# Performance work log

Hardware: AMD Instinct MI355X
Metric: run time of the kernel (lower is better)

The kernel has to match this reference:

```python
import jax, jax.numpy as jnp
import numpy as np

N = 20000          # n_nodes
E = 320000         # n_edges (before self loops)
F_IN, H1, H2 = 256, 64, 32
HEADS = 5
NEG_SLOPE = 0.2    # PyG GATConv leaky_relu default


def setup_inputs() -> dict:
    key = jax.random.key(0)
    ks = jax.random.split(key, 16)
    g = lambda i, shape, s: (jax.random.normal(ks[i], shape, jnp.float32) * s)
    inp = {
        "x": g(0, (N, F_IN), 1.0),
        "edge_index": jax.random.randint(ks[1], (2, E), 0, N, dtype=jnp.int32),
        "W1": g(2, (F_IN, HEADS * H1), 0.05),
        "att_src1": g(3, (HEADS, H1), 0.1),
        "att_dst1": g(4, (HEADS, H1), 0.1),
        "b1": jnp.zeros((H1,), jnp.float32),
        "W2": g(5, (H1, HEADS * H2), 0.1),
        "att_src2": g(6, (HEADS, H2), 0.1),
        "att_dst2": g(7, (HEADS, H2), 0.1),
        "b2": jnp.zeros((H2,), jnp.float32),
        "W3": g(8, (H1, HEADS * H2), 0.1),
        "att_src3": g(9, (HEADS, H2), 0.1),
        "att_dst3": g(10, (HEADS, H2), 0.1),
        "b3": jnp.zeros((H2,), jnp.float32),
    }
    return inp


def _add_self_loops(edge_index):
    loop = jnp.arange(N, dtype=edge_index.dtype)
    return jnp.concatenate([edge_index, jnp.stack([loop, loop])], axis=1)


def _gat_conv(x, edge_index, W, att_src, att_dst, b, act):
    # PyG GATConv, concat=False (mean over heads), add_self_loops already applied.
    heads, c = att_src.shape
    xw = (x @ W).reshape(N, heads, c)                     # [N,H,C]
    src, dst = edge_index[0], edge_index[1]               # messages src -> dst
    a_s = jnp.sum(xw * att_src, axis=-1)                  # [N,H]
    a_d = jnp.sum(xw * att_dst, axis=-1)                  # [N,H]
    e = jax.nn.leaky_relu(a_s[src] + a_d[dst], NEG_SLOPE) # [E',H]
    # scatter-softmax over edges sharing the same destination node
    m = jax.ops.segment_max(e, dst, num_segments=N)       # [N,H]
    e = jnp.exp(e - m[dst])
    denom = jax.ops.segment_sum(e, dst, num_segments=N)   # [N,H]
    alpha = e / (denom[dst] + 1e-16)                      # [E',H]
    # weighted scatter-aggregation of gathered source features
    out = jax.ops.segment_sum(alpha[:, :, None] * xw[src], dst, num_segments=N)
    out = out.mean(axis=1) + b                            # mean over heads, bias
    return act(out)


def reference(x, edge_index, W1, att_src1, att_dst1, b1,
              W2, att_src2, att_dst2, b2,
              W3, att_src3, att_dst3, b3):
    ei = _add_self_loops(edge_index)
    h1 = _gat_conv(x, ei, W1, att_src1, att_dst1, b1, jax.nn.relu)
    mu = _gat_conv(h1, ei, W2, att_src2, att_dst2, b2, lambda t: t)
    logvar = _gat_conv(h1, ei, W3, att_src3, att_dst3, b3, lambda t: t)
    z = mu  # eval-mode reparameterize: z = mu
    return (z, mu, logvar)
```

## Files before the change

### kernel.cpp

```cpp
#include <hip/hip_runtime.h>
#include <math.h>

#define N_NODES 20000
#define N_EDGES 320000
#define EP (N_EDGES + N_NODES)
#define HEADS 5

typedef __attribute__((ext_vector_type(8))) __bf16 bf16x8;
typedef __attribute__((ext_vector_type(4))) float f32x4;

__device__ __forceinline__ float lrelu(float s) { return (s > 0.f) ? s : 0.2f * s; }

__device__ __forceinline__ unsigned f2bf(float f) {
  unsigned u = __float_as_uint(f);
  return (u + 0x7fffu + ((u >> 16) & 1u)) >> 16;
}

__global__ void count_deg_k(const int* __restrict__ ei, int* __restrict__ deg) {
  int e = blockIdx.x * blockDim.x + threadIdx.x;
  if (e >= EP) return;
  int dst = (e < N_EDGES) ? ei[N_EDGES + e] : (e - N_EDGES);
  atomicAdd(&deg[dst], 1);
}

__global__ __launch_bounds__(256) void scan1_k(const int* __restrict__ deg,
                                               int* __restrict__ offs,
                                               int* __restrict__ bsum) {
  __shared__ int buf[256];
  int tid = threadIdx.x, i = blockIdx.x * 256 + tid;
  int v = (i < N_NODES) ? deg[i] : 0;
  buf[tid] = v;
  __syncthreads();
  for (int o = 1; o < 256; o <<= 1) {
    int t = (tid >= o) ? buf[tid - o] : 0;
    __syncthreads();
    buf[tid] += t;
    __syncthreads();
  }
  if (i < N_NODES) offs[i] = buf[tid] - v;
  if (tid == 255) bsum[blockIdx.x] = buf[255];
}

__global__ __launch_bounds__(128) void scan2_k(int* __restrict__ bsum, int nb) {
  __shared__ int buf[128];
  int tid = threadIdx.x;
  int v = (tid < nb) ? bsum[tid] : 0;
  buf[tid] = v;
  __syncthreads();
  for (int o = 1; o < 128; o <<= 1) {
    int t = (tid >= o) ? buf[tid - o] : 0;
    __syncthreads();
    buf[tid] += t;
    __syncthreads();
  }
  if (tid < nb) bsum[tid] = buf[tid] - v;
}

__global__ void scan3_k(int* __restrict__ offs, const int* __restrict__ bsum) {
  int i = blockIdx.x * 256 + threadIdx.x;
  if (i < N_NODES) offs[i] += bsum[blockIdx.x];
  if (i == 0) offs[N_NODES] = EP;
}

__global__ void scatter_k(const int* __restrict__ ei, const int* __restrict__ offs,
                          int* __restrict__ cursor, int* __restrict__ ssrc) {
  int e = blockIdx.x * blockDim.x + threadIdx.x;
  if (e >= EP) return;
  int src, dst;
  if (e < N_EDGES) { src = ei[e]; dst = ei[N_EDGES + e]; }
  else             { src = e - N_EDGES; dst = src; }
  int pos = atomicAdd(&cursor[dst], 1);
  ssrc[offs[dst] + pos] = src;
}

__global__ __launch_bounds__(256) void conv_bf16_k(const float4* __restrict__ src,
                                                   uint2* __restrict__ dst, int n4) {
  int t = blockIdx.x * blockDim.x + threadIdx.x;
  if (t >= n4) return;
  float4 v = src[t];
  unsigned p0 = f2bf(v.x) | (f2bf(v.y) << 16);
  unsigned p1 = f2bf(v.z) | (f2bf(v.w) << 16);
  dst[t] = make_uint2(p0, p1);
}

__global__ void packW1_k(const float* __restrict__ W, unsigned short* __restrict__ Wp) {
  int t = blockIdx.x * blockDim.x + threadIdx.x;
  if (t >= 256 * 320) return;
  int k = t / 320, n = t % 320;
  int gnt = n >> 4, ll = n & 15;
  int ks = k >> 5, kr = k & 31;
  int lh = kr >> 3, i = kr & 7;
  Wp[(((size_t)gnt * 8 + ks) * 64 + lh * 16 + ll) * 8 + i] = (unsigned short)f2bf(W[t]);
}

__global__ void packW23_k(const float* __restrict__ W2, const float* __restrict__ W3,
                          unsigned short* __restrict__ Wp) {
  int t = blockIdx.x * blockDim.x + threadIdx.x;
  if (t >= 64 * 320) return;
  int k = t / 320, n = t % 320;
  int u = n / 32, c = n % 32;
  float val = (u < HEADS) ? W2[k * 160 + u * 32 + c] : W3[k * 160 + (u - HEADS) * 32 + c];
  int gnt = n >> 4, ll = n & 15;
  int ks = k >> 5, kr = k & 31;
  int lh = kr >> 3, i = kr & 7;
  Wp[(((size_t)gnt * 2 + ks) * 64 + lh * 16 + ll) * 8 + i] = (unsigned short)f2bf(val);
}

template <int KSTEPS, int CH>
__global__ __launch_bounds__(256) void mfma_gemm_k(
    const unsigned short* __restrict__ A, const unsigned short* __restrict__ Bp,
    unsigned short* __restrict__ Cb,
    const float* __restrict__ attAs, const float* __restrict__ attAd,
    const float* __restrict__ attBs, const float* __restrict__ attBd,
    float* __restrict__ as_out, float* __restrict__ ad_out, int M) {
  constexpr int K = KSTEPS * 32;
  int panel = blockIdx.x;
  int bm = blockIdx.y * 64;
  int w = threadIdx.x >> 6;
  int l = threadIdx.x & 63;
  int ll = l & 15, lh = l >> 4;

  int arow = bm + w * 16 + ll;
  if (arow >= M) arow = M - 1;
  const unsigned short* ap = A + (size_t)arow * K + lh * 8;

  f32x4 acc[4] = {};
  for (int ks = 0; ks < KSTEPS; ks++) {
    bf16x8 af = *(const bf16x8*)(ap + ks * 32);
#pragma unroll
    for (int nt = 0; nt < 4; nt++) {
      bf16x8 bf = *(const bf16x8*)(Bp + (((size_t)(panel * 4 + nt) * KSTEPS + ks) * 64 + l) * 8);
      acc[nt] = __builtin_amdgcn_mfma_f32_16x16x32_bf16(af, bf, acc[nt], 0, 0, 0);
    }
  }

  int row0 = bm + w * 16 + lh * 4;
#pragma unroll
  for (int j = 0; j < 4; j++) {
    int r = row0 + j;
    if (r < M) {
#pragma unroll
      for (int nt = 0; nt < 4; nt++)
        Cb[((size_t)panel * M + r) * 64 + nt * 16 + ll] = (unsigned short)f2bf(acc[nt][j]);
    }
  }

  float ws[4], wd[4];
  if (CH == 64) {
#pragma unroll
    for (int nt = 0; nt < 4; nt++) {
      ws[nt] = attAs[panel * 64 + nt * 16 + ll];
      wd[nt] = attAd[panel * 64 + nt * 16 + ll];
    }
  } else {
#pragma unroll
    for (int nt = 0; nt < 4; nt++) {
      int u = panel * 2 + (nt >> 1);
      int c = (nt & 1) * 16 + ll;
      const float* s = (u < HEADS) ? attAs + u * 32 : attBs + (u - HEADS) * 32;
      const float* d = (u < HEADS) ? attAd + u * 32 : attBd + (u - HEADS) * 32;
      ws[nt] = s[c]; wd[nt] = d[c];
    }
  }
#pragma unroll
  for (int j = 0; j < 4; j++) {
    int r = row0 + j;
    if (CH == 64) {
      float ps = acc[0][j] * ws[0] + acc[1][j] * ws[1] + acc[2][j] * ws[2] + acc[3][j] * ws[3];
      float pd = acc[0][j] * wd[0] + acc[1][j] * wd[1] + acc[2][j] * wd[2] + acc[3][j] * wd[3];
#pragma unroll
      for (int o = 1; o < 16; o <<= 1) {
        ps += __shfl_xor(ps, o);
        pd += __shfl_xor(pd, o);
      }
      if (ll == 0 && r < M) {
        as_out[(size_t)panel * M + r] = ps;
        ad_out[(size_t)panel * M + r] = pd;
      }
    } else {
      float ls = acc[0][j] * ws[0] + acc[1][j] * ws[1];
      float ld = acc[0][j] * wd[0] + acc[1][j] * wd[1];
      float hs = acc[2][j] * ws[2] + acc[3][j] * ws[3];
      float hd = acc[2][j] * wd[2] + acc[3][j] * wd[3];
#pragma unroll
      for (int o = 1; o < 16; o <<= 1) {
        ls += __shfl_xor(ls, o); ld += __shfl_xor(ld, o);
        hs += __shfl_xor(hs, o); hd += __shfl_xor(hd, o);
      }
      if (ll == 0 && r < M) {
        int ulo = panel * 2, uhi = panel * 2 + 1;
        as_out[(size_t)ulo * M + r] = ls;  ad_out[(size_t)ulo * M + r] = ld;
        as_out[(size_t)uhi * M + r] = hs;  ad_out[(size_t)uhi * M + r] = hd;
      }
    }
  }
}

__device__ __forceinline__ void bf4(uint2 v, float& f0, float& f1, float& f2, float& f3) {
  f0 = __uint_as_float(v.x << 16);
  f1 = __uint_as_float(v.x & 0xffff0000u);
  f2 = __uint_as_float(v.y << 16);
  f3 = __uint_as_float(v.y & 0xffff0000u);
}

__global__ __launch_bounds__(320) void agg1_k(const int* __restrict__ offs,
                                              const int* __restrict__ ssrc,
                                              const float* __restrict__ a_s,
                                              const float* __restrict__ a_d,
                                              const uint2* __restrict__ xwb,
                                              const float* __restrict__ b1,
                                              unsigned short* __restrict__ h1b) {
  int n = blockIdx.x;
  int u = threadIdx.x >> 6;
  int lane = threadIdx.x & 63;
  int off = offs[n], end = offs[n + 1];
  int deg = end - off;
  float ad = a_d[(size_t)u * N_NODES + n];
  const float* asl = a_s + (size_t)u * N_NODES;
  const uint2* xb  = xwb + (size_t)u * N_NODES * 16;
  int g = lane >> 4, q = lane & 15;
  float ax = 0.f, ay = 0.f, az = 0.f, aw = 0.f;

  __shared__ uint2 eLds[HEADS][64];
  __shared__ float sacc[HEADS][64];

  if (deg <= 64) {
    int s = 0;
    float e = -1e30f;
    if (lane < deg) { s = ssrc[off + lane]; e = lrelu(asl[s] + ad); }
    float m = e;
#pragma unroll
    for (int o = 32; o > 0; o >>= 1) m = fmaxf(m, __shfl_xor(m, o));
    float p = (lane < deg) ? __expf(e - m) : 0.f;
    float den = p;
#pragma unroll
    for (int o = 32; o > 0; o >>= 1) den += __shfl_xor(den, o);
    float alpha = p * (1.f / (den + 1e-16f));

    eLds[u][lane] = make_uint2(__float_as_uint(alpha), (unsigned)s);

    for (int base = 0; base < deg; base += 16) {
      float alv[4];
      uint2 v[4];
#pragma unroll
      for (int t = 0; t < 4; t++) {
        int b4 = base + t * 4;
        if (b4 < deg) {
          uint2 es = eLds[u][b4 + g];
          alv[t] = __uint_as_float(es.x);
          v[t] = xb[(size_t)es.y * 16 + q];
        }
      }
#pragma unroll
      for (int t = 0; t < 4; t++) {
        if (base + t * 4 < deg) {
          float f0, f1, f2, f3;
          bf4(v[t], f0, f1, f2, f3);
          ax += alv[t] * f0; ay += alv[t] * f1;
          az += alv[t] * f2; aw += alv[t] * f3;
        }
      }
    }
  } else {
    float m = -1e30f;
    for (int i = off + lane; i < end; i += 64) m = fmaxf(m, lrelu(asl[ssrc[i]] + ad));
#pragma unroll
    for (int o = 32; o > 0; o >>= 1) m = fmaxf(m, __shfl_xor(m, o));
    float den = 0.f;
    for (int i = off + lane; i < end; i += 64) den += __expf(lrelu(asl[ssrc[i]] + ad) - m);
#pragma unroll
    for (int o = 32; o > 0; o >>= 1) den += __shfl_xor(den, o);
    float inv = 1.f / (den + 1e-16f);
    for (int base = off; base < end; base += 4) {
      int e = base + g;
      if (e < end) {
        int sv = ssrc[e];
        float al = __expf(lrelu(asl[sv] + ad) - m) * inv;
        float f0, f1, f2, f3;
        bf4(xb[(size_t)sv * 16 + q], f0, f1, f2, f3);
        ax += al * f0; ay += al * f1; az += al * f2; aw += al * f3;
      }
    }
  }

#pragma unroll
  for (int o = 16; o < 64; o <<= 1) {
    ax += __shfl_xor(ax, o); ay += __shfl_xor(ay, o);
    az += __shfl_xor(az, o); aw += __shfl_xor(aw, o);
  }

  if (g == 0) *(float4*)&sacc[u][q * 4] = make_float4(ax, ay, az, aw);
  __syncthreads();
  if (threadIdx.x < 64) {
    int t = threadIdx.x;
    float v = sacc[0][t] + sacc[1][t] + sacc[2][t] + sacc[3][t] + sacc[4][t];
    v = fmaxf(v * 0.2f + b1[t], 0.f);
    h1b[(size_t)n * 64 + t] = (unsigned short)f2bf(v);
  }
}

__global__ __launch_bounds__(320) void agg23_k(const int* __restrict__ offs,
                                               const int* __restrict__ ssrc,
                                               const float* __restrict__ a_s,
                                               const float* __restrict__ a_d,
                                               const uint2* __restrict__ xwb,
                                               const float* __restrict__ b2,
                                               const float* __restrict__ b3,
                                               float* __restrict__ z_out,
                                               float* __restrict__ mu_out,
                                               float* __restrict__ lv_out) {
  int n = blockIdx.x;
  int gp = threadIdx.x >> 6;
  int lane = threadIdx.x & 63;
  int ulo = 2 * gp, uhi = 2 * gp + 1;
  int off = offs[n], end = offs[n + 1];
  int deg = end - off;
  float adlo = a_d[(size_t)ulo * N_NODES + n];
  float adhi = a_d[(size_t)uhi * N_NODES + n];
  const float* aslo = a_s + (size_t)ulo * N_NODES;
  const float* ashi = a_s + (size_t)uhi * N_NODES;
  const uint2* xb   = xwb + (size_t)gp * N_NODES * 16;
  int g = lane >> 4, q = lane & 15;
  float ax = 0.f, ay = 0.f, az = 0.f, aw = 0.f;

  __shared__ uint4 eLds[HEADS][64];
  __shared__ float sacc[HEADS][2][32];

  if (deg <= 64) {
    int s = 0;
    float elo = -1e30f, ehi = -1e30f;
    if (lane < deg) {
      s = ssrc[off + lane];
      elo = lrelu(aslo[s] + adlo);
      ehi = lrelu(ashi[s] + adhi);
    }
    float mlo = elo, mhi = ehi;
#pragma unroll
    for (int o = 32; o > 0; o >>= 1) {
      mlo = fmaxf(mlo, __shfl_xor(mlo, o));
      mhi = fmaxf(mhi, __shfl_xor(mhi, o));
    }
    float plo = (lane < deg) ? __expf(elo - mlo) : 0.f;
    float phi = (lane < deg) ? __expf(ehi - mhi) : 0.f;
    float dlo = plo, dhi = phi;
#pragma unroll
    for (int o = 32; o > 0; o >>= 1) {
      dlo += __shfl_xor(dlo, o);
      dhi += __shfl_xor(dhi, o);
    }
    float allo = plo * (1.f / (dlo + 1e-16f));
    float alhi = phi * (1.f / (dhi + 1e-16f));

    eLds[gp][lane] = make_uint4(__float_as_uint(allo), __float_as_uint(alhi),
                                (unsigned)s, 0u);

    for (int base = 0; base < deg; base += 16) {
      float alv[4];
      uint2 v[4];
#pragma unroll
      for (int t = 0; t < 4; t++) {
        int b4 = base + t * 4;
        if (b4 < deg) {
          uint4 es = eLds[gp][b4 + g];
          alv[t] = __uint_as_float((q < 8) ? es.x : es.y);
          v[t] = xb[(size_t)es.z * 16 + q];
        }
      }
#pragma unroll
      for (int t = 0; t < 4; t++) {
        if (base + t * 4 < deg) {
          float f0, f1, f2, f3;
          bf4(v[t], f0, f1, f2, f3);
          ax += alv[t] * f0; ay += alv[t] * f1;
          az += alv[t] * f2; aw += alv[t] * f3;
        }
      }
    }
  } else {
    float mlo = -1e30f, mhi = -1e30f;
    for (int i = off + lane; i < end; i += 64) {
      int sv = ssrc[i];
      mlo = fmaxf(mlo, lrelu(aslo[sv] + adlo));
      mhi = fmaxf(mhi, lrelu(ashi[sv] + adhi));
    }
#pragma unroll
    for (int o = 32; o > 0; o >>= 1) {
      mlo = fmaxf(mlo, __shfl_xor(mlo, o));
      mhi = fmaxf(mhi, __shfl_xor(mhi, o));
    }
    float dlo = 0.f, dhi = 0.f;
    for (int i = off + lane; i < end; i += 64) {
      int sv = ssrc[i];
      dlo += __expf(lrelu(aslo[sv] + adlo) - mlo);
      dhi += __expf(lrelu(ashi[sv] + adhi) - mhi);
    }
#pragma unroll
    for (int o = 32; o > 0; o >>= 1) {
      dlo += __shfl_xor(dlo, o);
      dhi += __shfl_xor(dhi, o);
    }
    float ilo = 1.f / (dlo + 1e-16f), ihi = 1.f / (dhi + 1e-16f);
    for (int base = off; base < end; base += 4) {
      int e = base + g;
      if (e < end) {
        int sv = ssrc[e];
        float al;
        if (q < 8) al = __expf(lrelu(aslo[sv] + adlo) - mlo) * ilo;
        else       al = __expf(lrelu(ashi[sv] + adhi) - mhi) * ihi;
        float f0, f1, f2, f3;
        bf4(xb[(size_t)sv * 16 + q], f0, f1, f2, f3);
        ax += al * f0; ay += al * f1; az += al * f2; aw += al * f3;
      }
    }
  }

#pragma unroll
  for (int o = 16; o < 64; o <<= 1) {
    ax += __shfl_xor(ax, o); ay += __shfl_xor(ay, o);
    az += __shfl_xor(az, o); aw += __shfl_xor(aw, o);
  }

  if (g == 0)
    *(float4*)&sacc[gp][q >> 3][(q & 7) * 4] = make_float4(ax, ay, az, aw);
  __syncthreads();
  if (threadIdx.x < 64) {
    int t = threadIdx.x;
    if (t < 32) {
      float v = sacc[0][0][t] + sacc[0][1][t] + sacc[1][0][t] + sacc[1][1][t] + sacc[2][0][t];
      v = v * 0.2f + b2[t];
      z_out[(size_t)n * 32 + t]  = v;
      mu_out[(size_t)n * 32 + t] = v;
    } else {
      int c = t - 32;
      float v = sacc[2][1][c] + sacc[3][0][c] + sacc[3][1][c] + sacc[4][0][c] + sacc[4][1][c];
      v = v * 0.2f + b3[c];
      lv_out[(size_t)n * 32 + c] = v;
    }
  }
}

extern "C" void kernel_launch(void* const* d_in, const int* in_sizes, int n_in,
                              void* d_out, int out_size, void* d_ws, size_t ws_size,
                              hipStream_t stream) {
  const float* x        = (const float*)d_in[0];
  const int*   ei       = (const int*)d_in[1];
  const float* W1       = (const float*)d_in[2];
  const float* att_src1 = (const float*)d_in[3];
  const float* att_dst1 = (const float*)d_in[4];
  const float* b1       = (const float*)d_in[5];
  const float* W2       = (const float*)d_in[6];
  const float* att_src2 = (const float*)d_in[7];
  const float* att_dst2 = (const float*)d_in[8];
  const float* b2       = (const float*)d_in[9];
  const float* W3       = (const float*)d_in[10];
  const float* att_src3 = (const float*)d_in[11];
  const float* att_dst3 = (const float*)d_in[12];
  const float* b3       = (const float*)d_in[13];
  float* out = (float*)d_out;

  char* w = (char*)d_ws;
  auto alloc = [&](size_t bytes) -> void* {
    void* p = (void*)w;
    w += (bytes + 255) & ~(size_t)255;
    return p;
  };
  int*            deg    = (int*)alloc((size_t)N_NODES * 4);
  int*            offs   = (int*)alloc((size_t)(N_NODES + 1) * 4);
  int*            cursor = (int*)alloc((size_t)N_NODES * 4);
  int*            bsum   = (int*)alloc((size_t)128 * 4);
  int*            ssrc   = (int*)alloc((size_t)EP * 4);
  unsigned short* xwb    = (unsigned short*)alloc((size_t)N_NODES * 320 * 2);
  float*          a_s    = (float*)alloc((size_t)N_NODES * 10 * 4);
  float*          a_d    = (float*)alloc((size_t)N_NODES * 10 * 4);
  unsigned short* h1b    = (unsigned short*)alloc((size_t)N_NODES * 64 * 2);
  unsigned short* xbf    = (unsigned short*)alloc((size_t)N_NODES * 256 * 2);
  unsigned short* Wp1    = (unsigned short*)alloc((size_t)256 * 320 * 2);
  unsigned short* Wp23   = (unsigned short*)alloc((size_t)64 * 320 * 2);

  hipMemsetAsync(deg, 0, (size_t)N_NODES * 4, stream);
  hipMemsetAsync(cursor, 0, (size_t)N_NODES * 4, stream);

  int eb = (EP + 255) / 256;
  int nb = (N_NODES + 255) / 256;
  count_deg_k<<<eb, 256, 0, stream>>>(ei, deg);
  scan1_k<<<nb, 256, 0, stream>>>(deg, offs, bsum);
  scan2_k<<<1, 128, 0, stream>>>(bsum, nb);
  scan3_k<<<nb, 256, 0, stream>>>(offs, bsum);
  scatter_k<<<eb, 256, 0, stream>>>(ei, offs, cursor, ssrc);

  int nx4 = N_NODES * 256 / 4;
  conv_bf16_k<<<(nx4 + 255) / 256, 256, 0, stream>>>((const float4*)x, (uint2*)xbf, nx4);
  packW1_k<<<(256 * 320 + 255) / 256, 256, 0, stream>>>(W1, Wp1);
  packW23_k<<<(64 * 320 + 255) / 256, 256, 0, stream>>>(W2, W3, Wp23);

  dim3 gg(5, 313);

  mfma_gemm_k<8, 64><<<gg, 256, 0, stream>>>(xbf, Wp1, xwb,
                                             att_src1, att_dst1, nullptr, nullptr,
                                             a_s, a_d, N_NODES);
  agg1_k<<<N_NODES, 320, 0, stream>>>(offs, ssrc, a_s, a_d, (const uint2*)xwb, b1, h1b);

  mfma_gemm_k<2, 32><<<gg, 256, 0, stream>>>(h1b, Wp23, xwb,
                                             att_src2, att_dst2, att_src3, att_dst3,
                                             a_s, a_d, N_NODES);
  agg23_k<<<N_NODES, 320, 0, stream>>>(offs, ssrc, a_s, a_d, (const uint2*)xwb, b2, b3,
                                       out, out + (size_t)N_NODES * 32,
                                       out + (size_t)2 * N_NODES * 32);
}
```

Measured before the change: 200.0 us.

## Split per-node aggregation into per-head wave work items plus separate reduction kernels

The aggregation kernels now use one wavefront per (head, node) pair in 256-thread blocks, indexed head-major. Each wave writes its partial sums to a global buffer, and new reduction kernels sum the five heads and apply bias, activation and output conversion. This drops the block-wide __syncthreads and the 320-thread blocks, so a node with a high in-degree no longer holds back the other heads, and head-major order may improve gather locality. The cost is a global round trip for the partials (N×320 floats), two extra launches, and the partial buffer now aliases the bf16 x buffer.

```diff
diff --git a/kernel.cpp b/kernel.cpp
--- a/kernel.cpp
+++ b/kernel.cpp
@@ -203,16 +203,17 @@
   f3 = __uint_as_float(v.y & 0xffff0000u);
 }
 
-__global__ __launch_bounds__(320) void agg1_k(const int* __restrict__ offs,
-                                              const int* __restrict__ ssrc,
-                                              const float* __restrict__ a_s,
-                                              const float* __restrict__ a_d,
-                                              const uint2* __restrict__ xwb,
-                                              const float* __restrict__ b1,
-                                              unsigned short* __restrict__ h1b) {
-  int n = blockIdx.x;
-  int u = threadIdx.x >> 6;
+__global__ __launch_bounds__(256) void agg1u_k(const int* __restrict__ offs,
+                                               const int* __restrict__ ssrc,
+                                               const float* __restrict__ a_s,
+                                               const float* __restrict__ a_d,
+                                               const uint2* __restrict__ xwb,
+                                               float* __restrict__ part) {
+  int wid = blockIdx.x * 4 + (threadIdx.x >> 6);
   int lane = threadIdx.x & 63;
+  if (wid >= N_NODES * HEADS) return;
+  int u = wid / N_NODES, n = wid - u * N_NODES;
+  int w4 = threadIdx.x >> 6;
   int off = offs[n], end = offs[n + 1];
   int deg = end - off;
   float ad = a_d[(size_t)u * N_NODES + n];
@@ -221,8 +222,7 @@
   int g = lane >> 4, q = lane & 15;
   float ax = 0.f, ay = 0.f, az = 0.f, aw = 0.f;
 
-  __shared__ uint2 eLds[HEADS][64];
-  __shared__ float sacc[HEADS][64];
+  __shared__ uint2 eLds[4][64];
 
   if (deg <= 64) {
     int s = 0;
@@ -237,7 +237,7 @@
     for (int o = 32; o > 0; o >>= 1) den += __shfl_xor(den, o);
     float alpha = p * (1.f / (den + 1e-16f));
 
-    eLds[u][lane] = make_uint2(__float_as_uint(alpha), (unsigned)s);
+    eLds[w4][lane] = make_uint2(__float_as_uint(alpha), (unsigned)s);
 
     for (int base = 0; base < deg; base += 16) {
       float alv[4];
@@ -246,7 +246,7 @@
       for (int t = 0; t < 4; t++) {
         int b4 = base + t * 4;
         if (b4 < deg) {
-          uint2 es = eLds[u][b4 + g];
+          uint2 es = eLds[w4][b4 + g];
           alv[t] = __uint_as_float(es.x);
           v[t] = xb[(size_t)es.y * 16 + q];
         }
@@ -288,30 +288,44 @@
     ax += __shfl_xor(ax, o); ay += __shfl_xor(ay, o);
     az += __shfl_xor(az, o); aw += __shfl_xor(aw, o);
   }
-
-  if (g == 0) *(float4*)&sacc[u][q * 4] = make_float4(ax, ay, az, aw);
-  __syncthreads();
-  if (threadIdx.x < 64) {
-    int t = threadIdx.x;
-    float v = sacc[0][t] + sacc[1][t] + sacc[2][t] + sacc[3][t] + sacc[4][t];
-    v = fmaxf(v * 0.2f + b1[t], 0.f);
-    h1b[(size_t)n * 64 + t] = (unsigned short)f2bf(v);
-  }
-}
-
-__global__ __launch_bounds__(320) void agg23_k(const int* __restrict__ offs,
-                                               const int* __restrict__ ssrc,
-                                               const float* __restrict__ a_s,
-                                               const float* __restrict__ a_d,
-                                               const uint2* __restrict__ xwb,
-                                               const float* __restrict__ b2,
-                                               const float* __restrict__ b3,
-                                               float* __restrict__ z_out,
-                                               float* __restrict__ mu_out,
-                                               float* __restrict__ lv_out) {
-  int n = blockIdx.x;
-  int gp = threadIdx.x >> 6;
+  if (g == 0)
+    *(float4*)&part[((size_t)u * N_NODES + n) * 64 + q * 4] =
+        make_float4(ax, ay, az, aw);
+}
+
+__global__ __launch_bounds__(256) void red1_k(const float* __restrict__ part,
+                                              const float* __restrict__ b1,
+                                              unsigned short* __restrict__ h1b) {
+  int t = blockIdx.x * blockDim.x + threadIdx.x;
+  if (t >= N_NODES * 16) return;
+  int n = t >> 4, q = t & 15;
+  float x = 0.f, y = 0.f, z = 0.f, w = 0.f;
+#pragma unroll
+  for (int h = 0; h < HEADS; h++) {
+    float4 v = *(const float4*)&part[((size_t)h * N_NODES + n) * 64 + q * 4];
+    x += v.x; y += v.y; z += v.z; w += v.w;
+  }
+  float4 bb = *(const float4*)&b1[q * 4];
+  unsigned short r0 = (unsigned short)f2bf(fmaxf(x * 0.2f + bb.x, 0.f));
+  unsigned short r1 = (unsigned short)f2bf(fmaxf(y * 0.2f + bb.y, 0.f));
+  unsigned short r2 = (unsigned short)f2bf(fmaxf(z * 0.2f + bb.z, 0.f));
+  unsigned short r3 = (unsigned short)f2bf(fmaxf(w * 0.2f + bb.w, 0.f));
+  unsigned p0 = (unsigned)r0 | ((unsigned)r1 << 16);
+  unsigned p1 = (unsigned)r2 | ((unsigned)r3 << 16);
+  *(uint2*)&h1b[(size_t)n * 64 + q * 4] = make_uint2(p0, p1);
+}
+
+__global__ __launch_bounds__(256) void agg23u_k(const int* __restrict__ offs,
+                                                const int* __restrict__ ssrc,
+                                                const float* __restrict__ a_s,
+                                                const float* __restrict__ a_d,
+                                                const uint2* __restrict__ xwb,
+                                                float* __restrict__ part) {
+  int wid = blockIdx.x * 4 + (threadIdx.x >> 6);
   int lane = threadIdx.x & 63;
+  if (wid >= N_NODES * HEADS) return;
+  int gp = wid / N_NODES, n = wid - gp * N_NODES;
+  int w4 = threadIdx.x >> 6;
   int ulo = 2 * gp, uhi = 2 * gp + 1;
   int off = offs[n], end = offs[n + 1];
   int deg = end - off;
@@ -323,8 +337,7 @@
   int g = lane >> 4, q = lane & 15;
   float ax = 0.f, ay = 0.f, az = 0.f, aw = 0.f;
 
-  __shared__ uint4 eLds[HEADS][64];
-  __shared__ float sacc[HEADS][2][32];
+  __shared__ uint4 eLds[4][64];
 
   if (deg <= 64) {
     int s = 0;
@@ -351,7 +364,7 @@
     float allo = plo * (1.f / (dlo + 1e-16f));
     float alhi = phi * (1.f / (dhi + 1e-16f));
 
-    eLds[gp][lane] = make_uint4(__float_as_uint(allo), __float_as_uint(alhi),
+    eLds[w4][lane] = make_uint4(__float_as_uint(allo), __float_as_uint(alhi),
                                 (unsigned)s, 0u);
 
     for (int base = 0; base < deg; base += 16) {
@@ -361,7 +374,7 @@
       for (int t = 0; t < 4; t++) {
         int b4 = base + t * 4;
         if (b4 < deg) {
-          uint4 es = eLds[gp][b4 + g];
+          uint4 es = eLds[w4][b4 + g];
           alv[t] = __uint_as_float((q < 8) ? es.x : es.y);
           v[t] = xb[(size_t)es.z * 16 + q];
         }
@@ -419,24 +432,40 @@
     ax += __shfl_xor(ax, o); ay += __shfl_xor(ay, o);
     az += __shfl_xor(az, o); aw += __shfl_xor(aw, o);
   }
-
   if (g == 0)
-    *(float4*)&sacc[gp][q >> 3][(q & 7) * 4] = make_float4(ax, ay, az, aw);
-  __syncthreads();
-  if (threadIdx.x < 64) {
-    int t = threadIdx.x;
-    if (t < 32) {
-      float v = sacc[0][0][t] + sacc[0][1][t] + sacc[1][0][t] + sacc[1][1][t] + sacc[2][0][t];
-      v = v * 0.2f + b2[t];
-      z_out[(size_t)n * 32 + t]  = v;
-      mu_out[(size_t)n * 32 + t] = v;
-    } else {
-      int c = t - 32;
-      float v = sacc[2][1][c] + sacc[3][0][c] + sacc[3][1][c] + sacc[4][0][c] + sacc[4][1][c];
-      v = v * 0.2f + b3[c];
-      lv_out[(size_t)n * 32 + c] = v;
-    }
-  }
+    *(float4*)&part[((size_t)gp * N_NODES + n) * 64 + q * 4] =
+        make_float4(ax, ay, az, aw);
+}
+
+__global__ __launch_bounds__(256) void red23_k(const float* __restrict__ part,
+                                               const float* __restrict__ b2,
+                                               const float* __restrict__ b3,
+                                               float* __restrict__ z_out,
+                                               float* __restrict__ mu_out,
+                                               float* __restrict__ lv_out) {
+  int t = blockIdx.x * blockDim.x + threadIdx.x;
+  if (t >= N_NODES * 8) return;
+  int n = t >> 3, q = t & 7;
+  int c = q * 4;
+  auto P = [&](int g, int j) -> float4 {
+    return *(const float4*)&part[((size_t)g * N_NODES + n) * 64 + j];
+  };
+  float4 a0 = P(0, c), a1 = P(0, 32 + c), a2 = P(1, c), a3 = P(1, 32 + c), a4 = P(2, c);
+  float4 l0 = P(2, 32 + c), l1 = P(3, c), l2 = P(3, 32 + c), l3 = P(4, c), l4 = P(4, 32 + c);
+  float4 bb2 = *(const float4*)&b2[c];
+  float4 bb3 = *(const float4*)&b3[c];
+  float4 o2, o3;
+  o2.x = (a0.x + a1.x + a2.x + a3.x + a4.x) * 0.2f + bb2.x;
+  o2.y = (a0.y + a1.y + a2.y + a3.y + a4.y) * 0.2f + bb2.y;
+  o2.z = (a0.z + a1.z + a2.z + a3.z + a4.z) * 0.2f + bb2.z;
+  o2.w = (a0.w + a1.w + a2.w + a3.w + a4.w) * 0.2f + bb2.w;
+  o3.x = (l0.x + l1.x + l2.x + l3.x + l4.x) * 0.2f + bb3.x;
+  o3.y = (l0.y + l1.y + l2.y + l3.y + l4.y) * 0.2f + bb3.y;
+  o3.z = (l0.z + l1.z + l2.z + l3.z + l4.z) * 0.2f + bb3.z;
+  o3.w = (l0.w + l1.w + l2.w + l3.w + l4.w) * 0.2f + bb3.w;
+  *(float4*)&z_out[(size_t)n * 32 + c]  = o2;
+  *(float4*)&mu_out[(size_t)n * 32 + c] = o2;
+  *(float4*)&lv_out[(size_t)n * 32 + c] = o3;
 }
 
 extern "C" void kernel_launch(void* const* d_in, const int* in_sizes, int n_in,
@@ -473,9 +502,10 @@
   float*          a_s    = (float*)alloc((size_t)N_NODES * 10 * 4);
   float*          a_d    = (float*)alloc((size_t)N_NODES * 10 * 4);
   unsigned short* h1b    = (unsigned short*)alloc((size_t)N_NODES * 64 * 2);
-  unsigned short* xbf    = (unsigned short*)alloc((size_t)N_NODES * 256 * 2);
   unsigned short* Wp1    = (unsigned short*)alloc((size_t)256 * 320 * 2);
   unsigned short* Wp23   = (unsigned short*)alloc((size_t)64 * 320 * 2);
+  float*          part   = (float*)alloc((size_t)N_NODES * 320 * 4);
+  unsigned short* xbf    = (unsigned short*)part;
 
   hipMemsetAsync(deg, 0, (size_t)N_NODES * 4, stream);
   hipMemsetAsync(cursor, 0, (size_t)N_NODES * 4, stream);
@@ -494,16 +524,19 @@
   packW23_k<<<(64 * 320 + 255) / 256, 256, 0, stream>>>(W2, W3, Wp23);
 
   dim3 gg(5, 313);
+  int aggb = (N_NODES * HEADS + 3) / 4;
 
   mfma_gemm_k<8, 64><<<gg, 256, 0, stream>>>(xbf, Wp1, xwb,
                                              att_src1, att_dst1, nullptr, nullptr,
                                              a_s, a_d, N_NODES);
-  agg1_k<<<N_NODES, 320, 0, stream>>>(offs, ssrc, a_s, a_d, (const uint2*)xwb, b1, h1b);
+  agg1u_k<<<aggb, 256, 0, stream>>>(offs, ssrc, a_s, a_d, (const uint2*)xwb, part);
+  red1_k<<<(N_NODES * 16 + 255) / 256, 256, 0, stream>>>(part, b1, h1b);
 
   mfma_gemm_k<2, 32><<<gg, 256, 0, stream>>>(h1b, Wp23, xwb,
                                              att_src2, att_dst2, att_src3, att_dst3,
                                              a_s, a_d, N_NODES);
-  agg23_k<<<N_NODES, 320, 0, stream>>>(offs, ssrc, a_s, a_d, (const uint2*)xwb, b2, b3,
-                                       out, out + (size_t)N_NODES * 32,
-                                       out + (size_t)2 * N_NODES * 32);
-}
+  agg23u_k<<<aggb, 256, 0, stream>>>(offs, ssrc, a_s, a_d, (const uint2*)xwb, part);
+  red23_k<<<(N_NODES * 8 + 255) / 256, 256, 0, stream>>>(part, b2, b3,
+                                                         out, out + (size_t)N_NODES * 32,
+                                                         out + (size_t)2 * N_NODES * 32);
+}
```

Measured after the change: 195.8 us. -2.1%, faster.
